# Kernel optimization log

Hardware: AMD Instinct MI355X
Metric: run time of the kernel (lower is better)

The kernel has to match this reference:

```python
import math
import jax, jax.numpy as jnp
import numpy as np

INPUT_DIM = 1024
HEADS = 16
SEQ = 4096
BATCH = 1
SCALE = math.sqrt(INPUT_DIM / HEADS)  # 8.0


def setup_inputs() -> dict:
    key = jax.random.key(0)
    ks = jax.random.split(key, 5)
    D = INPUT_DIM
    return {
        "x": jax.random.normal(ks[0], (BATCH, SEQ, D), dtype=jnp.float32),
        "w_qkv": jax.random.normal(ks[1], (3 * D, D), dtype=jnp.float32) * (1.0 / math.sqrt(D)),
        "b_qkv": jax.random.normal(ks[2], (3 * D,), dtype=jnp.float32) * 0.01,
        "w_out": jax.random.normal(ks[3], (D, D), dtype=jnp.float32) * (1.0 / math.sqrt(D)),
        "b_out": jax.random.normal(ks[4], (D,), dtype=jnp.float32) * 0.01,
    }


def reference(x, w_qkv, b_qkv, w_out, b_out):
    b, n, D = x.shape
    h = HEADS
    d = D // h
    # qkv projection: [b, n, 3D]
    qkv = x @ w_qkv.T + b_qkv
    # 'b n (c h d) -> b c h n d' with c=3 outermost
    qkv = qkv.reshape(b, n, 3, h, d).transpose(2, 0, 3, 1, 4)  # [3, b, h, n, d]
    q, k, v = qkv[0], qkv[1], qkv[2]
    q = q / SCALE
    attn = jnp.einsum('bhnd,bhmd->bhnm', q, k)  # [b, h, n, n]
    attn = jax.nn.softmax(attn, axis=-1)
    # dropout is identity in eval mode
    context = jnp.einsum('bhnm,bhmd->bhnd', attn, v)  # [b, h, n, d]
    context = context.transpose(0, 2, 1, 3).reshape(b, n, D)  # 'b h n d -> b n (h d)'
    return context @ w_out.T + b_out
```

## Files before the change

kernel.cpp:

```cpp
#include <hip/hip_runtime.h>

typedef unsigned short u16;
typedef unsigned int u32;
typedef __attribute__((ext_vector_type(8))) short short8;
typedef __attribute__((ext_vector_type(4))) float f32x4;

__device__ __forceinline__ u16 f2b(float f) {
  union { float f; unsigned u; } v; v.f = f;
  unsigned r = (v.u + 0x7FFFu + ((v.u >> 16) & 1u)) >> 16;
  return (u16)r;
}
__device__ __forceinline__ float b2f(u16 b) {
  union { unsigned u; float f; } v; v.u = ((unsigned)b) << 16;
  return v.f;
}
__device__ __forceinline__ u32 cvtpk(float a, float b) {
  u32 r;
  asm("v_cvt_pk_bf16_f32 %0, %1, %2" : "=v"(r) : "v"(a), "v"(b));
  return r;
}
__device__ __forceinline__ void p32swap(u32& a, u32& b) {
  asm("v_permlane32_swap_b32 %0, %1" : "+v"(a), "+v"(b));
}
__device__ __forceinline__ void p16swap(u32& a, u32& b) {
  asm("v_permlane16_swap_b32 %0, %1" : "+v"(a), "+v"(b));
}
__device__ __forceinline__ float ldf(const void* p, size_t i, int f32) {
  return f32 ? ((const float*)p)[i] : b2f(((const u16*)p)[i]);
}

__global__ __launch_bounds__(256) void detect_dtype(const u16* __restrict__ x,
                                                    int* __restrict__ flag) {
  __shared__ int cnt;
  if (threadIdx.x == 0) cnt = 0;
  __syncthreads();
  int local = 0;
  for (int p = threadIdx.x; p < 512; p += 256) {
    int e = (x[2 * p] >> 7) & 0xFF;
    if (e >= 0xC0) local++;
  }
  atomicAdd(&cnt, local);
  __syncthreads();
  if (threadIdx.x == 0) flag[0] = (cnt >= 16) ? 1 : 0;
}

__global__ __launch_bounds__(256) void convert_all(
    const void* __restrict__ px, const void* __restrict__ pwq,
    const void* __restrict__ pbq, const void* __restrict__ pwo,
    const void* __restrict__ pbo, u16* __restrict__ xb,
    u16* __restrict__ wqkvb, u16* __restrict__ bqkvb, u16* __restrict__ wob,
    u16* __restrict__ bob) {
  __shared__ int sf;
  if (threadIdx.x == 0) sf = 0;
  __syncthreads();
  {
    const u16* xr = (const u16*)px;
    int local = 0;
    for (int p = threadIdx.x; p < 512; p += 256) {
      int e = (xr[2 * p] >> 7) & 0xFF;
      if (e >= 0xC0) local++;
    }
    atomicAdd(&sf, local);
  }
  __syncthreads();
  const int isf32 = (sf >= 16);

  int i = blockIdx.x * 256 + threadIdx.x;
  const void* in; u16* out; size_t g;
  if (i < 524288)       { in = px;  out = xb;    g = (size_t)i; }
  else if (i < 917504)  { in = pwq; out = wqkvb; g = (size_t)(i - 524288); }
  else if (i < 917888)  { in = pbq; out = bqkvb; g = (size_t)(i - 917504); }
  else if (i < 1048960) { in = pwo; out = wob;   g = (size_t)(i - 917888); }
  else                  { in = pbo; out = bob;   g = (size_t)(i - 1048960); }
  size_t base = g * 8;
  if (isf32) {
    const float* p = (const float*)in + base;
    float4 v0 = *(const float4*)p, v1 = *(const float4*)(p + 4);
    union { short8 v; u16 e[8]; } t;
    t.e[0]=f2b(v0.x); t.e[1]=f2b(v0.y); t.e[2]=f2b(v0.z); t.e[3]=f2b(v0.w);
    t.e[4]=f2b(v1.x); t.e[5]=f2b(v1.y); t.e[6]=f2b(v1.z); t.e[7]=f2b(v1.w);
    *(short8*)(out + base) = t.v;
  } else {
    *(short8*)(out + base) = *(const short8*)((const u16*)in + base);
  }
}

__global__ __launch_bounds__(256) void transpose_v(const u16* __restrict__ qkv,
                                                   u16* __restrict__ Vt) {
  __shared__ u16 T[64 * 72];
  const int tid = threadIdx.x;
  const int h = blockIdx.y;
  const int s0 = blockIdx.x * 64;
  for (int r = 0; r < 2; ++r) {
    int cid = r * 256 + tid;
    int s = cid >> 3, c8 = cid & 7;
    union { short8 v; u16 u[8]; } uu;
    uu.v = *(const short8*)(qkv + (size_t)(s0 + s) * 3072 + 2048 + h * 64 + c8 * 8);
    for (int i = 0; i < 8; ++i) T[(c8 * 8 + i) * 72 + s] = uu.u[i];
  }
  __syncthreads();
  for (int r = 0; r < 2; ++r) {
    int cid = r * 256 + tid;
    int dd = cid >> 3, c8 = cid & 7;
    union { short8 v; u16 u[8]; } uu;
    for (int i = 0; i < 8; ++i) uu.u[i] = T[dd * 72 + c8 * 8 + i];
    *(short8*)(Vt + (size_t)(h * 64 + dd) * 4096 + s0 + c8 * 8) = uu.v;
  }
}

__global__ __launch_bounds__(256) void gemm1_db(const u16* __restrict__ A,
                                                const u16* __restrict__ B,
                                                const u16* __restrict__ bias,
                                                u16* __restrict__ C,
                                                int K, int lda, int ldb, int ldc) {
  __shared__ __align__(16) u16 sm[2][16384];
  const int tid = threadIdx.x;
  const int w = tid >> 6, lane = tid & 63;
  const int lq = lane & 15, qr = lane >> 4;
  const int m0 = blockIdx.y * 128, n0 = blockIdx.x * 128;
  const int wm = (w >> 1) * 64, wn = (w & 1) * 64;

  f32x4 acc[4][4];
  for (int i = 0; i < 4; i++)
    for (int j = 0; j < 4; j++) acc[i][j] = (f32x4){0.f, 0.f, 0.f, 0.f};
  float bv[4];
  for (int ns = 0; ns < 4; ++ns) bv[ns] = b2f(bias[n0 + wn + ns * 16 + lq]);

  const int rs = tid >> 3, cs = tid & 7;
  const u16* gA = A + (size_t)(m0 + rs) * lda + cs * 8;
  const u16* gB = B + (size_t)(n0 + rs) * ldb + cs * 8;
  const int lofs = (tid & ~63) << 3;

#define GSTAGE(buf, k0)                                                      \
  do {                                                                       \
    u16* As_ = &sm[buf][0];                                                  \
    u16* Bs_ = &sm[buf][8192];                                               \
    for (int r = 0; r < 4; ++r) {                                            \
      __builtin_amdgcn_global_load_lds(gA + (size_t)(r * 32) * lda + (k0),   \
                                       As_ + lofs + r * 2048, 16, 0, 0);     \
      __builtin_amdgcn_global_load_lds(gB + (size_t)(r * 32) * ldb + (k0),   \
                                       Bs_ + lofs + r * 2048, 16, 0, 0);     \
    }                                                                        \
  } while (0)

  GSTAGE(0, 0);
  __syncthreads();

  const int nk = K >> 6;
  for (int kt = 0; kt < nk; ++kt) {
    const int cur = kt & 1;
    if (kt + 1 < nk) GSTAGE(cur ^ 1, (kt + 1) * 64);
    const u16* As = &sm[cur][0];
    const u16* Bs = &sm[cur][8192];
    for (int ks = 0; ks < 2; ++ks) {
      short8 af[4], bf[4];
      const int sw = ks * 4 + qr;
      for (int i = 0; i < 4; i++) {
        af[i] = *(const short8*)(As + (wm + i * 16 + lq) * 64 + sw * 8);
        bf[i] = *(const short8*)(Bs + (wn + i * 16 + lq) * 64 + sw * 8);
      }
      for (int mi = 0; mi < 4; mi++)
        for (int ni = 0; ni < 4; ni++)
          acc[mi][ni] = __builtin_amdgcn_mfma_f32_16x16x32_bf16(
              af[mi], bf[ni], acc[mi][ni], 0, 0, 0);
    }
    __syncthreads();
  }
#undef GSTAGE

  u16* SH = &sm[0][0];
  for (int mi = 0; mi < 4; mi++)
    for (int ni = 0; ni < 4; ni++)
      for (int r = 0; r < 4; ++r)
        SH[(wm + mi * 16 + qr * 4 + r) * 132 + wn + ni * 16 + lq] =
            f2b(acc[mi][ni][r] + bv[ni]);
  __syncthreads();
  for (int it = 0; it < 8; ++it) {
    int idx = it * 256 + tid;
    int row = idx >> 4, c8 = idx & 15;
    *(short8*)(C + (size_t)(m0 + row) * ldc + n0 + c8 * 8) =
        *(const short8*)(SH + row * 132 + c8 * 8);
  }
}

__global__ __launch_bounds__(256) void gemm_bt(const void* __restrict__ A,
                                               const void* __restrict__ B,
                                               const void* __restrict__ bias,
                                               void* __restrict__ C,
                                               int M, int N, int K,
                                               int lda, int ldb, int ldc,
                                               int aMay, int bMay, int outF32,
                                               const int* __restrict__ flag) {
  __shared__ __align__(16) u16 sm[128 * 132];
  u16* As = sm;
  u16* Bs = sm + 128 * 64;
  const int f = flag[0];
  const int a32 = aMay && f, b32 = bMay && f;
  const int tid = threadIdx.x;
  const int w = tid >> 6, lane = tid & 63;
  const int lq = lane & 15, qr = lane >> 4;
  const int m0 = blockIdx.y * 128, n0 = blockIdx.x * 128;
  const int wm = (w >> 1) * 64, wn = (w & 1) * 64;

  f32x4 acc[4][4];
  for (int i = 0; i < 4; i++)
    for (int j = 0; j < 4; j++) acc[i][j] = (f32x4){0.f, 0.f, 0.f, 0.f};
  float bv[4];
  for (int ns = 0; ns < 4; ++ns) bv[ns] = ldf(bias, n0 + wn + ns * 16 + lq, b32);

  const int rs = tid >> 3, cs = tid & 7;
  const u16* gA = (const u16*)A + (size_t)(m0 + rs) * lda + cs * 8;
  const u16* gB = (const u16*)B + (size_t)(n0 + rs) * ldb + cs * 8;
  u16* lA = As + ((tid & ~63) << 3);
  u16* lB = Bs + ((tid & ~63) << 3);

  for (int k0 = 0; k0 < K; k0 += 64) {
    if (!(a32 | b32)) {
      for (int r = 0; r < 4; ++r) {
        __builtin_amdgcn_global_load_lds(gA + (size_t)(r * 32) * lda + k0,
                                         lA + r * 2048, 16, 0, 0);
        __builtin_amdgcn_global_load_lds(gB + (size_t)(r * 32) * ldb + k0,
                                         lB + r * 2048, 16, 0, 0);
      }
    } else {
      for (int r = 0; r < 4; ++r) {
        int cid = r * 256 + tid;
        int row = cid >> 3, c = cid & 7;
        if (a32) {
          const float* p = (const float*)A + (size_t)(m0 + row) * lda + k0 + c * 8;
          float4 v0 = *(const float4*)p, v1 = *(const float4*)(p + 4);
          union { short8 v; u16 e[8]; } t;
          t.e[0]=f2b(v0.x); t.e[1]=f2b(v0.y); t.e[2]=f2b(v0.z); t.e[3]=f2b(v0.w);
          t.e[4]=f2b(v1.x); t.e[5]=f2b(v1.y); t.e[6]=f2b(v1.z); t.e[7]=f2b(v1.w);
          *(short8*)(As + row * 64 + c * 8) = t.v;
        } else {
          *(short8*)(As + row * 64 + c * 8) =
              *(const short8*)((const u16*)A + (size_t)(m0 + row) * lda + k0 + c * 8);
        }
        if (b32) {
          const float* p = (const float*)B + (size_t)(n0 + row) * ldb + k0 + c * 8;
          float4 v0 = *(const float4*)p, v1 = *(const float4*)(p + 4);
          union { short8 v; u16 e[8]; } t;
          t.e[0]=f2b(v0.x); t.e[1]=f2b(v0.y); t.e[2]=f2b(v0.z); t.e[3]=f2b(v0.w);
          t.e[4]=f2b(v1.x); t.e[5]=f2b(v1.y); t.e[6]=f2b(v1.z); t.e[7]=f2b(v1.w);
          *(short8*)(Bs + row * 64 + c * 8) = t.v;
        } else {
          *(short8*)(Bs + row * 64 + c * 8) =
              *(const short8*)((const u16*)B + (size_t)(n0 + row) * ldb + k0 + c * 8);
        }
      }
    }
    __syncthreads();
    for (int ks = 0; ks < 2; ++ks) {
      short8 af[4], bf[4];
      const int sw = ks * 4 + qr;
      for (int i = 0; i < 4; i++) {
        af[i] = *(const short8*)(As + (wm + i * 16 + lq) * 64 + sw * 8);
        bf[i] = *(const short8*)(Bs + (wn + i * 16 + lq) * 64 + sw * 8);
      }
      for (int mi = 0; mi < 4; mi++)
        for (int ni = 0; ni < 4; ni++)
          acc[mi][ni] = __builtin_amdgcn_mfma_f32_16x16x32_bf16(
              af[mi], bf[ni], acc[mi][ni], 0, 0, 0);
    }
    __syncthreads();
  }

  if (!outF32) {
    u16* SH = sm;
    for (int mi = 0; mi < 4; mi++)
      for (int ni = 0; ni < 4; ni++)
        for (int r = 0; r < 4; ++r)
          SH[(wm + mi * 16 + qr * 4 + r) * 132 + wn + ni * 16 + lq] =
              f2b(acc[mi][ni][r] + bv[ni]);
    __syncthreads();
    for (int it = 0; it < 8; ++it) {
      int idx = it * 256 + tid;
      int row = idx >> 4, c8 = idx & 15;
      *(short8*)((u16*)C + (size_t)(m0 + row) * ldc + n0 + c8 * 8) =
          *(const short8*)(SH + row * 132 + c8 * 8);
    }
  } else {
    float* Cf = (float*)C;
    for (int mi = 0; mi < 4; mi++) {
      int row = m0 + wm + mi * 16 + qr * 4;
      for (int r = 0; r < 4; ++r) {
        float* rp = Cf + (size_t)(row + r) * ldc + n0 + wn;
        for (int ni = 0; ni < 4; ni++)
          rp[ni * 16 + lq] = acc[mi][ni][r] + bv[ni];
      }
    }
  }
}

__global__ __launch_bounds__(512, 2) void gemm_bt_ks(const u16* __restrict__ A,
                                                     const u16* __restrict__ B,
                                                     const u16* __restrict__ bias,
                                                     float* __restrict__ C,
                                                     int K, int lda, int ldb, int ldc) {
  __shared__ __align__(16) u16 sm[2][16384];
  const int tid = threadIdx.x;
  const int w = tid >> 6, lane = tid & 63;
  const int half = w >> 2, wq = w & 3;
  const int ht = tid & 255;
  const int lq = lane & 15, qr = lane >> 4;
  const int m0 = blockIdx.y * 128, n0 = blockIdx.x * 128;
  const int wm = (wq >> 1) * 64, wn = (wq & 1) * 64;
  const int kh = K >> 1;

  u16* As = &sm[half][0];
  u16* Bs = &sm[half][8192];

  f32x4 acc[4][4];
  for (int i = 0; i < 4; i++)
    for (int j = 0; j < 4; j++) acc[i][j] = (f32x4){0.f, 0.f, 0.f, 0.f};
  float bv[4];
  for (int ns = 0; ns < 4; ++ns) bv[ns] = b2f(bias[n0 + wn + ns * 16 + lq]);

  const int rs = ht >> 3, cs = ht & 7;
  const u16* gA = A + (size_t)(m0 + rs) * lda + half * kh + cs * 8;
  const u16* gB = B + (size_t)(n0 + rs) * ldb + half * kh + cs * 8;
  u16* lA = As + ((ht & ~63) << 3);
  u16* lB = Bs + ((ht & ~63) << 3);

  for (int k0 = 0; k0 < kh; k0 += 64) {
    for (int r = 0; r < 4; ++r) {
      __builtin_amdgcn_global_load_lds(gA + (size_t)(r * 32) * lda + k0,
                                       lA + r * 2048, 16, 0, 0);
      __builtin_amdgcn_global_load_lds(gB + (size_t)(r * 32) * ldb + k0,
                                       lB + r * 2048, 16, 0, 0);
    }
    __syncthreads();
    for (int ks = 0; ks < 2; ++ks) {
      short8 af[4], bf[4];
      const int sw = ks * 4 + qr;
      for (int i = 0; i < 4; i++) {
        af[i] = *(const short8*)(As + (wm + i * 16 + lq) * 64 + sw * 8);
        bf[i] = *(const short8*)(Bs + (wn + i * 16 + lq) * 64 + sw * 8);
      }
      for (int mi = 0; mi < 4; mi++)
        for (int ni = 0; ni < 4; ni++)
          acc[mi][ni] = __builtin_amdgcn_mfma_f32_16x16x32_bf16(
              af[mi], bf[ni], acc[mi][ni], 0, 0, 0);
    }
    __syncthreads();
  }

  float* CB = (float*)&sm[0][0];
  float* p = CB + (size_t)ht * 33;
  for (int t = 0; t < 2; ++t) {
    if (half == 1) {
      for (int u = 0; u < 2; ++u)
        for (int ni = 0; ni < 4; ++ni)
          for (int r = 0; r < 4; ++r)
            p[u * 16 + ni * 4 + r] = acc[2 * t + u][ni][r];
    }
    __syncthreads();
    if (half == 0) {
      for (int u = 0; u < 2; ++u)
        for (int ni = 0; ni < 4; ++ni)
          for (int r = 0; r < 4; ++r)
            acc[2 * t + u][ni][r] += p[u * 16 + ni * 4 + r];
    }
    __syncthreads();
  }

  if (half == 0) {
    for (int mi = 0; mi < 4; mi++) {
      int row = m0 + wm + mi * 16 + qr * 4;
      for (int r = 0; r < 4; ++r) {
        float* rp = C + (size_t)(row + r) * ldc + n0 + wn;
        for (int ni = 0; ni < 4; ni++)
          rp[ni * 16 + lq] = acc[mi][ni][r] + bv[ni];
      }
    }
  }
}

__global__ __launch_bounds__(512, 2) void attn_split(const u16* __restrict__ qkv,
                                                     const u16* __restrict__ Vtg,
                                                     u16* __restrict__ ctx, int ldctx) {
  __shared__ __align__(16) u16 SMEM[2][16384];
  const int tid = threadIdx.x;
  const int w = tid >> 6, lane = tid & 63;
  const int half = w >> 2, wq = w & 3, wl = w & 3;
  const int lq = lane & 15, qr = lane >> 4;
  const int qb = blockIdx.x, h = blockIdx.y;
  const int qbase = qb * 128 + wq * 32;
  const float cs = 0.18033688011112042f;

  short8 qf[2][2];
#pragma unroll
  for (int mi = 0; mi < 2; ++mi)
#pragma unroll
    for (int ks = 0; ks < 2; ++ks)
      qf[mi][ks] = *(const short8*)(qkv + (size_t)(qbase + mi * 16 + lq) * 3072 +
                                    h * 64 + ks * 32 + qr * 8);

  f32x4 o[2][4];
#pragma unroll
  for (int mi = 0; mi < 2; ++mi)
#pragma unroll
    for (int ds = 0; ds < 4; ++ds) o[mi][ds] = (f32x4){0.f, 0.f, 0.f, 0.f};
  float lrow[2] = {0.f, 0.f};

  const int csw = ((lane & 7) ^ (lane >> 3)) << 3;
  const int r0v = wl * 8 + (lane >> 3);
  const u16* sK0 = qkv + (size_t)(half * 2048 + r0v) * 3072 + 1024 + h * 64 + csw;
  const u16* sK1 = sK0 + (size_t)32 * 3072;
  const u16* sV0 = Vtg + (size_t)(h * 64 + r0v) * 4096 + half * 2048 + csw;
  const u16* sV1 = sV0 + (size_t)32 * 4096;
  const int kb = half * 4096 + wl * 512;
  const int vb = 8192 + half * 4096 + wl * 512;

#define STAGE(buf)                                                          \
  do {                                                                      \
    u16* B_ = &SMEM[buf][0];                                                \
    __builtin_amdgcn_global_load_lds(sK0, B_ + kb, 16, 0, 0);               \
    __builtin_amdgcn_global_load_lds(sK1, B_ + kb + 2048, 16, 0, 0);        \
    __builtin_amdgcn_global_load_lds(sV0, B_ + vb, 16, 0, 0);               \
    __builtin_amdgcn_global_load_lds(sV1, B_ + vb + 2048, 16, 0, 0);        \
    sK0 += (size_t)64 * 3072; sK1 += (size_t)64 * 3072;                     \
    sV0 += 64; sV1 += 64;                                                   \
  } while (0)

  STAGE(0);
  __syncthreads();

  for (int it = 0; it < 32; ++it) {
    const int cur = it & 1;
    if (it + 1 < 32) STAGE(cur ^ 1);
    const u16* Kh = &SMEM[cur][half * 4096];
    const u16* Vh = &SMEM[cur][8192 + half * 4096];

    f32x4 s[2][4];
#pragma unroll
    for (int mi = 0; mi < 2; ++mi)
#pragma unroll
      for (int ns = 0; ns < 4; ++ns) s[mi][ns] = (f32x4){0.f, 0.f, 0.f, 0.f};
#pragma unroll
    for (int ks = 0; ks < 2; ++ks) {
      short8 kf[4];
#pragma unroll
      for (int ns = 0; ns < 4; ++ns) {
        int rk = ns * 16 + lq;
        kf[ns] = *(const short8*)(Kh + rk * 64 + (((ks * 4 + qr) ^ (lq & 7)) << 3));
      }
      __builtin_amdgcn_s_setprio(1);
#pragma unroll
      for (int mi = 0; mi < 2; ++mi)
#pragma unroll
        for (int ns = 0; ns < 4; ++ns)
          s[mi][ns] = __builtin_amdgcn_mfma_f32_16x16x32_bf16(
              kf[ns], qf[mi][ks], s[mi][ns], 0, 0, 0);
      __builtin_amdgcn_s_setprio(0);
    }

    short8 pf[2][2];
#pragma unroll
    for (int mi = 0; mi < 2; ++mi) {
      float lacc = 0.f;
      u32 X[4], Y[4];
#pragma unroll
      for (int ns = 0; ns < 4; ++ns) {
        float p0 = __builtin_amdgcn_exp2f(fmaf(s[mi][ns][0], cs, -12.0f));
        float p1 = __builtin_amdgcn_exp2f(fmaf(s[mi][ns][1], cs, -12.0f));
        float p2 = __builtin_amdgcn_exp2f(fmaf(s[mi][ns][2], cs, -12.0f));
        float p3 = __builtin_amdgcn_exp2f(fmaf(s[mi][ns][3], cs, -12.0f));
        lacc += (p0 + p1) + (p2 + p3);
        X[ns] = cvtpk(p0, p1);
        Y[ns] = cvtpk(p2, p3);
      }
      lrow[mi] += lacc;
#pragma unroll
      for (int ks = 0; ks < 2; ++ks) {
        u32 a0 = X[2 * ks], b0 = X[2 * ks + 1];
        u32 a1 = Y[2 * ks], b1 = Y[2 * ks + 1];
        p32swap(a0, b0); p16swap(a0, b0);
        p32swap(a1, b1); p16swap(a1, b1);
        union { u32 u[4]; short8 v; } t;
        t.u[0] = a0; t.u[1] = a1; t.u[2] = b0; t.u[3] = b1;
        pf[mi][ks] = t.v;
      }
    }

#pragma unroll
    for (int ks = 0; ks < 2; ++ks) {
      short8 vf[4];
#pragma unroll
      for (int ds = 0; ds < 4; ++ds) {
        int dv = ds * 16 + lq;
        vf[ds] = *(const short8*)(Vh + (size_t)dv * 64 +
                                  (((ks * 4 + qr) ^ (lq & 7)) << 3));
      }
      __builtin_amdgcn_s_setprio(1);
#pragma unroll
      for (int mi = 0; mi < 2; ++mi)
#pragma unroll
        for (int ds = 0; ds < 4; ++ds)
          o[mi][ds] = __builtin_amdgcn_mfma_f32_16x16x32_bf16(
              vf[ds], pf[mi][ks], o[mi][ds], 0, 0, 0);
      __builtin_amdgcn_s_setprio(0);
    }
    __syncthreads();
  }
#undef STAGE

  float* CB = (float*)&SMEM[0][0];
#pragma unroll
  for (int mi = 0; mi < 2; ++mi) {
    float* p = CB + (size_t)(wq * 64 + lane) * 17;
    if (half == 1) {
#pragma unroll
      for (int ds = 0; ds < 4; ++ds) {
        p[ds * 4 + 0] = o[mi][ds][0];
        p[ds * 4 + 1] = o[mi][ds][1];
        p[ds * 4 + 2] = o[mi][ds][2];
        p[ds * 4 + 3] = o[mi][ds][3];
      }
      p[16] = lrow[mi];
    }
    __syncthreads();
    if (half == 0) {
#pragma unroll
      for (int ds = 0; ds < 4; ++ds) {
        o[mi][ds][0] += p[ds * 4 + 0];
        o[mi][ds][1] += p[ds * 4 + 1];
        o[mi][ds][2] += p[ds * 4 + 2];
        o[mi][ds][3] += p[ds * 4 + 3];
      }
      lrow[mi] += p[16];
    }
    __syncthreads();
  }

  if (half == 0) {
#pragma unroll
    for (int mi = 0; mi < 2; ++mi) {
      float l = lrow[mi];
      l += __shfl_xor(l, 16, 64);
      l += __shfl_xor(l, 32, 64);
      float linv = 1.f / fmaxf(l, 1e-30f);
      int row = qbase + mi * 16 + lq;
      u16* dst = ctx + (size_t)row * ldctx + h * 64 + qr * 4;
#pragma unroll
      for (int ds = 0; ds < 4; ++ds) {
        u32 lo = cvtpk(o[mi][ds][0] * linv, o[mi][ds][1] * linv);
        u32 hi = cvtpk(o[mi][ds][2] * linv, o[mi][ds][3] * linv);
        *(uint2*)(dst + ds * 16) = make_uint2(lo, hi);
      }
    }
  }
}

__global__ __launch_bounds__(256) void attn_fused(const u16* __restrict__ qkv,
                                                  const u16* __restrict__ Vtg,
                                                  u16* __restrict__ ctx, int ldctx) {
  __shared__ u16 Ks[64 * 64];
  __shared__ u16 Vts[64 * 64];
  const int tid = threadIdx.x;
  const int w = tid >> 6, lane = tid & 63;
  const int lq = lane & 15, qr = lane >> 4;
  const int qb = blockIdx.x, h = blockIdx.y;
  const int qbase = qb * 128 + w * 32;
  const float cs = 0.18033688011112042f;

  short8 qf[2][2];
  for (int mi = 0; mi < 2; ++mi)
    for (int ks = 0; ks < 2; ++ks)
      qf[mi][ks] = *(const short8*)(qkv + (size_t)(qbase + mi * 16 + lq) * 3072 +
                                    h * 64 + ks * 32 + qr * 8);

  f32x4 o[2][4];
  for (int mi = 0; mi < 2; ++mi)
    for (int ds = 0; ds < 4; ++ds) o[mi][ds] = (f32x4){0.f, 0.f, 0.f, 0.f};
  float lrow[2] = {0.f, 0.f};

  const int c = tid & 7, r0 = tid >> 3;
  u16* dKA = Ks + r0 * 64 + ((c ^ (r0 & 7)) << 3);
  u16* dKB = dKA + 32 * 64;
  const u16* sKA = qkv + (size_t)r0 * 3072 + 1024 + h * 64 + c * 8;
  const u16* sKB = sKA + (size_t)32 * 3072;
  const u16* sVfA = qkv + (size_t)r0 * 3072 + 2048 + h * 64 + c * 8;
  const u16* sVfB = sVfA + (size_t)32 * 3072;

  short8 rKA, rKB;
  union { short8 v; u16 e[8]; } ufA, ufB;
  rKA = *(const short8*)sKA; sKA += (size_t)64 * 3072;
  rKB = *(const short8*)sKB; sKB += (size_t)64 * 3072;
  ufA.v = *(const short8*)sVfA; sVfA += (size_t)64 * 3072;
  ufB.v = *(const short8*)sVfB; sVfB += (size_t)64 * 3072;

  for (int j0 = 0; j0 < 4096; j0 += 64) {
    __syncthreads();
    *(short8*)dKA = rKA;
    *(short8*)dKB = rKB;
    {
      const int jc = r0 >> 3;
      for (int i = 0; i < 8; ++i)
        Vts[(c * 8 + i) * 64 + ((jc ^ i) << 3) + (r0 & 7)] = ufA.e[i];
    }
    {
      const int jc = (r0 + 32) >> 3;
      for (int i = 0; i < 8; ++i)
        Vts[(c * 8 + i) * 64 + ((jc ^ i) << 3) + (r0 & 7)] = ufB.e[i];
    }
    __syncthreads();

    if (j0 + 64 < 4096) {
      rKA = *(const short8*)sKA; sKA += (size_t)64 * 3072;
      rKB = *(const short8*)sKB; sKB += (size_t)64 * 3072;
      ufA.v = *(const short8*)sVfA; sVfA += (size_t)64 * 3072;
      ufB.v = *(const short8*)sVfB; sVfB += (size_t)64 * 3072;
    }

    f32x4 s[2][4];
    for (int mi = 0; mi < 2; ++mi)
      for (int ns = 0; ns < 4; ++ns) s[mi][ns] = (f32x4){0.f, 0.f, 0.f, 0.f};
    for (int ks = 0; ks < 2; ++ks) {
      short8 kf[4];
      for (int ns = 0; ns < 4; ++ns) {
        int rk = ns * 16 + lq;
        kf[ns] = *(const short8*)(Ks + rk * 64 + (((ks * 4 + qr) ^ (lq & 7)) << 3));
      }
      __builtin_amdgcn_s_setprio(1);
      for (int mi = 0; mi < 2; ++mi)
        for (int ns = 0; ns < 4; ++ns)
          s[mi][ns] = __builtin_amdgcn_mfma_f32_16x16x32_bf16(
              kf[ns], qf[mi][ks], s[mi][ns], 0, 0, 0);
      __builtin_amdgcn_s_setprio(0);
    }

    short8 pf[2][2];
#pragma unroll
    for (int mi = 0; mi < 2; ++mi) {
      float lacc = 0.f;
      u32 X[4], Y[4];
#pragma unroll
      for (int ns = 0; ns < 4; ++ns) {
        float p0 = __builtin_amdgcn_exp2f(fmaf(s[mi][ns][0], cs, -12.0f));
        float p1 = __builtin_amdgcn_exp2f(fmaf(s[mi][ns][1], cs, -12.0f));
        float p2 = __builtin_amdgcn_exp2f(fmaf(s[mi][ns][2], cs, -12.0f));
        float p3 = __builtin_amdgcn_exp2f(fmaf(s[mi][ns][3], cs, -12.0f));
        lacc += (p0 + p1) + (p2 + p3);
        X[ns] = cvtpk(p0, p1);
        Y[ns] = cvtpk(p2, p3);
      }
      lrow[mi] += lacc;
#pragma unroll
      for (int ks = 0; ks < 2; ++ks) {
        u32 a0 = X[2 * ks], b0 = X[2 * ks + 1];
        u32 a1 = Y[2 * ks], b1 = Y[2 * ks + 1];
        p32swap(a0, b0); p16swap(a0, b0);
        p32swap(a1, b1); p16swap(a1, b1);
        union { u32 u[4]; short8 v; } t;
        t.u[0] = a0; t.u[1] = a1; t.u[2] = b0; t.u[3] = b1;
        pf[mi][ks] = t.v;
      }
    }

    for (int ks = 0; ks < 2; ++ks) {
      short8 vf[4];
      for (int ds = 0; ds < 4; ++ds) {
        int dv = ds * 16 + lq;
        vf[ds] = *(const short8*)(Vts + (size_t)dv * 64 +
                                  (((ks * 4 + qr) ^ (lq & 7)) << 3));
      }
      __builtin_amdgcn_s_setprio(1);
      for (int mi = 0; mi < 2; ++mi)
        for (int ds = 0; ds < 4; ++ds)
          o[mi][ds] = __builtin_amdgcn_mfma_f32_16x16x32_bf16(
              vf[ds], pf[mi][ks], o[mi][ds], 0, 0, 0);
      __builtin_amdgcn_s_setprio(0);
    }
  }

  for (int mi = 0; mi < 2; ++mi) {
    float l = lrow[mi];
    l += __shfl_xor(l, 16, 64);
    l += __shfl_xor(l, 32, 64);
    float linv = 1.f / fmaxf(l, 1e-30f);
    int row = qbase + mi * 16 + lq;
    u16* dst = ctx + (size_t)row * ldctx + h * 64 + qr * 4;
    for (int ds = 0; ds < 4; ++ds) {
      u32 lo = cvtpk(o[mi][ds][0] * linv, o[mi][ds][1] * linv);
      u32 hi = cvtpk(o[mi][ds][2] * linv, o[mi][ds][3] * linv);
      *(uint2*)(dst + ds * 16) = make_uint2(lo, hi);
    }
  }
}

extern "C" void kernel_launch(void* const* d_in, const int* in_sizes, int n_in,
                              void* d_out, int out_size, void* d_ws, size_t ws_size,
                              hipStream_t stream) {
  float* out = (float*)d_out;

  const void *px = nullptr, *pwq = nullptr, *pbq = nullptr, *pwo = nullptr, *pbo = nullptr;
  if (n_in == 5) {
    for (int i = 0; i < 5; ++i) {
      switch (in_sizes[i]) {
        case 4194304: px = d_in[i]; break;
        case 3145728: pwq = d_in[i]; break;
        case 3072:    pbq = d_in[i]; break;
        case 1048576: pwo = d_in[i]; break;
        case 1024:    pbo = d_in[i]; break;
        default: break;
      }
    }
  }
  if (!px || !pwq || !pbq || !pwo || !pbo) {
    px = d_in[0]; pwq = d_in[1]; pbq = d_in[2]; pwo = d_in[3]; pbo = d_in[4];
  }

  int* flag = (int*)d_ws;
  u16* qkv = (u16*)((char*)d_ws + 64);
  u16* ctx = qkv;

  const size_t nQKV = (size_t)4096 * 3072;
  const size_t nVt = (size_t)16 * 64 * 4096;
  const size_t nx = 4194304, nwq = 3145728, nwo = 1048576;
  u16* Vtg = qkv + nQKV;
  const size_t need_vt = 64 + (nQKV + nVt) * 2;
  const size_t need_full = need_vt + (nx + nwq + 4096 + nwo + 1024) * 2;

  if (ws_size >= need_full) {
    u16* xb    = Vtg + nVt;
    u16* wqkvb = xb + nx;
    u16* bqkvb = wqkvb + nwq;
    u16* wob   = bqkvb + 4096;
    u16* bob   = wob + nwo;
    convert_all<<<4098, 256, 0, stream>>>(px, pwq, pbq, pwo, pbo,
                                          xb, wqkvb, bqkvb, wob, bob);

    gemm1_db<<<dim3(24, 32), 256, 0, stream>>>(xb, wqkvb, bqkvb, qkv,
                                               1024, 1024, 1024, 3072);
    transpose_v<<<dim3(64, 16), 256, 0, stream>>>(qkv, Vtg);
    attn_split<<<dim3(32, 16), 512, 0, stream>>>(qkv, Vtg, ctx, 3072);
    gemm_bt_ks<<<dim3(8, 32), 512, 0, stream>>>(ctx, wob, bob, out,
                                                1024, 3072, 1024, 1024);
  } else if (ws_size >= need_vt) {
    detect_dtype<<<1, 256, 0, stream>>>((const u16*)px, flag);
    gemm_bt<<<dim3(24, 32), 256, 0, stream>>>(px, pwq, pbq, qkv,
                                              4096, 3072, 1024, 1024, 1024, 3072,
                                              1, 1, 0, flag);
    transpose_v<<<dim3(64, 16), 256, 0, stream>>>(qkv, Vtg);
    attn_split<<<dim3(32, 16), 512, 0, stream>>>(qkv, Vtg, ctx, 3072);
    gemm_bt<<<dim3(8, 32), 256, 0, stream>>>(ctx, pwo, pbo, out,
                                             4096, 1024, 1024, 3072, 1024, 1024,
                                             0, 1, 1, flag);
  } else {
    detect_dtype<<<1, 256, 0, stream>>>((const u16*)px, flag);
    gemm_bt<<<dim3(24, 32), 256, 0, stream>>>(px, pwq, pbq, qkv,
                                              4096, 3072, 1024, 1024, 1024, 3072,
                                              1, 1, 0, flag);
    attn_fused<<<dim3(32, 16), 256, 0, stream>>>(qkv, (const u16*)nullptr, ctx, 3072);
    gemm_bt<<<dim3(8, 32), 256, 0, stream>>>(ctx, pwo, pbo, out,
                                             4096, 1024, 1024, 3072, 1024, 1024,
                                             0, 1, 1, flag);
  }
}
```

Measured before the change: 244.6 us.

## Replace split-K output GEMM with double-buffered single-pass GEMM

Result: faster. 235.5 us (-3.7%).

```diff
diff --git a/kernel.cpp b/kernel.cpp
--- a/kernel.cpp
+++ b/kernel.cpp
@@ -180,6 +180,76 @@
     int row = idx >> 4, c8 = idx & 15;
     *(short8*)(C + (size_t)(m0 + row) * ldc + n0 + c8 * 8) =
         *(const short8*)(SH + row * 132 + c8 * 8);
+  }
+}
+
+__global__ __launch_bounds__(256) void gemm2_db(const u16* __restrict__ A,
+                                                const u16* __restrict__ B,
+                                                const u16* __restrict__ bias,
+                                                float* __restrict__ C,
+                                                int K, int lda, int ldb, int ldc) {
+  __shared__ __align__(16) u16 sm[2][16384];
+  const int tid = threadIdx.x;
+  const int w = tid >> 6, lane = tid & 63;
+  const int lq = lane & 15, qr = lane >> 4;
+  const int m0 = blockIdx.y * 128, n0 = blockIdx.x * 128;
+  const int wm = (w >> 1) * 64, wn = (w & 1) * 64;
+
+  f32x4 acc[4][4];
+  for (int i = 0; i < 4; i++)
+    for (int j = 0; j < 4; j++) acc[i][j] = (f32x4){0.f, 0.f, 0.f, 0.f};
+  float bv[4];
+  for (int ns = 0; ns < 4; ++ns) bv[ns] = b2f(bias[n0 + wn + ns * 16 + lq]);
+
+  const int rs = tid >> 3, cs = tid & 7;
+  const u16* gA = A + (size_t)(m0 + rs) * lda + cs * 8;
+  const u16* gB = B + (size_t)(n0 + rs) * ldb + cs * 8;
+  const int lofs = (tid & ~63) << 3;
+
+#define GSTAGE(buf, k0)                                                      \
+  do {                                                                       \
+    u16* As_ = &sm[buf][0];                                                  \
+    u16* Bs_ = &sm[buf][8192];                                               \
+    for (int r = 0; r < 4; ++r) {                                            \
+      __builtin_amdgcn_global_load_lds(gA + (size_t)(r * 32) * lda + (k0),   \
+                                       As_ + lofs + r * 2048, 16, 0, 0);     \
+      __builtin_amdgcn_global_load_lds(gB + (size_t)(r * 32) * ldb + (k0),   \
+                                       Bs_ + lofs + r * 2048, 16, 0, 0);     \
+    }                                                                        \
+  } while (0)
+
+  GSTAGE(0, 0);
+  __syncthreads();
+
+  const int nk = K >> 6;
+  for (int kt = 0; kt < nk; ++kt) {
+    const int cur = kt & 1;
+    if (kt + 1 < nk) GSTAGE(cur ^ 1, (kt + 1) * 64);
+    const u16* As = &sm[cur][0];
+    const u16* Bs = &sm[cur][8192];
+    for (int ks = 0; ks < 2; ++ks) {
+      short8 af[4], bf[4];
+      const int sw = ks * 4 + qr;
+      for (int i = 0; i < 4; i++) {
+        af[i] = *(const short8*)(As + (wm + i * 16 + lq) * 64 + sw * 8);
+        bf[i] = *(const short8*)(Bs + (wn + i * 16 + lq) * 64 + sw * 8);
+      }
+      for (int mi = 0; mi < 4; mi++)
+        for (int ni = 0; ni < 4; ni++)
+          acc[mi][ni] = __builtin_amdgcn_mfma_f32_16x16x32_bf16(
+              af[mi], bf[ni], acc[mi][ni], 0, 0, 0);
+    }
+    __syncthreads();
+  }
+#undef GSTAGE
+
+  for (int mi = 0; mi < 4; mi++) {
+    int row = m0 + wm + mi * 16 + qr * 4;
+    for (int r = 0; r < 4; ++r) {
+      float* rp = C + (size_t)(row + r) * ldc + n0 + wn;
+      for (int ni = 0; ni < 4; ni++)
+        rp[ni * 16 + lq] = acc[mi][ni][r] + bv[ni];
+    }
   }
 }
 
@@ -293,90 +363,6 @@
   }
 }
 
-__global__ __launch_bounds__(512, 2) void gemm_bt_ks(const u16* __restrict__ A,
-                                                     const u16* __restrict__ B,
-                                                     const u16* __restrict__ bias,
-                                                     float* __restrict__ C,
-                                                     int K, int lda, int ldb, int ldc) {
-  __shared__ __align__(16) u16 sm[2][16384];
-  const int tid = threadIdx.x;
-  const int w = tid >> 6, lane = tid & 63;
-  const int half = w >> 2, wq = w & 3;
-  const int ht = tid & 255;
-  const int lq = lane & 15, qr = lane >> 4;
-  const int m0 = blockIdx.y * 128, n0 = blockIdx.x * 128;
-  const int wm = (wq >> 1) * 64, wn = (wq & 1) * 64;
-  const int kh = K >> 1;
-
-  u16* As = &sm[half][0];
-  u16* Bs = &sm[half][8192];
-
-  f32x4 acc[4][4];
-  for (int i = 0; i < 4; i++)
-    for (int j = 0; j < 4; j++) acc[i][j] = (f32x4){0.f, 0.f, 0.f, 0.f};
-  float bv[4];
-  for (int ns = 0; ns < 4; ++ns) bv[ns] = b2f(bias[n0 + wn + ns * 16 + lq]);
-
-  const int rs = ht >> 3, cs = ht & 7;
-  const u16* gA = A + (size_t)(m0 + rs) * lda + half * kh + cs * 8;
-  const u16* gB = B + (size_t)(n0 + rs) * ldb + half * kh + cs * 8;
-  u16* lA = As + ((ht & ~63) << 3);
-  u16* lB = Bs + ((ht & ~63) << 3);
-
-  for (int k0 = 0; k0 < kh; k0 += 64) {
-    for (int r = 0; r < 4; ++r) {
-      __builtin_amdgcn_global_load_lds(gA + (size_t)(r * 32) * lda + k0,
-                                       lA + r * 2048, 16, 0, 0);
-      __builtin_amdgcn_global_load_lds(gB + (size_t)(r * 32) * ldb + k0,
-                                       lB + r * 2048, 16, 0, 0);
-    }
-    __syncthreads();
-    for (int ks = 0; ks < 2; ++ks) {
-      short8 af[4], bf[4];
-      const int sw = ks * 4 + qr;
-      for (int i = 0; i < 4; i++) {
-        af[i] = *(const short8*)(As + (wm + i * 16 + lq) * 64 + sw * 8);
-        bf[i] = *(const short8*)(Bs + (wn + i * 16 + lq) * 64 + sw * 8);
-      }
-      for (int mi = 0; mi < 4; mi++)
-        for (int ni = 0; ni < 4; ni++)
-          acc[mi][ni] = __builtin_amdgcn_mfma_f32_16x16x32_bf16(
-              af[mi], bf[ni], acc[mi][ni], 0, 0, 0);
-    }
-    __syncthreads();
-  }
-
-  float* CB = (float*)&sm[0][0];
-  float* p = CB + (size_t)ht * 33;
-  for (int t = 0; t < 2; ++t) {
-    if (half == 1) {
-      for (int u = 0; u < 2; ++u)
-        for (int ni = 0; ni < 4; ++ni)
-          for (int r = 0; r < 4; ++r)
-            p[u * 16 + ni * 4 + r] = acc[2 * t + u][ni][r];
-    }
-    __syncthreads();
-    if (half == 0) {
-      for (int u = 0; u < 2; ++u)
-        for (int ni = 0; ni < 4; ++ni)
-          for (int r = 0; r < 4; ++r)
-            acc[2 * t + u][ni][r] += p[u * 16 + ni * 4 + r];
-    }
-    __syncthreads();
-  }
-
-  if (half == 0) {
-    for (int mi = 0; mi < 4; mi++) {
-      int row = m0 + wm + mi * 16 + qr * 4;
-      for (int r = 0; r < 4; ++r) {
-        float* rp = C + (size_t)(row + r) * ldc + n0 + wn;
-        for (int ni = 0; ni < 4; ni++)
-          rp[ni * 16 + lq] = acc[mi][ni][r] + bv[ni];
-      }
-    }
-  }
-}
-
 __global__ __launch_bounds__(512, 2) void attn_split(const u16* __restrict__ qkv,
                                                      const u16* __restrict__ Vtg,
                                                      u16* __restrict__ ctx, int ldctx) {
@@ -736,8 +722,8 @@
                                                1024, 1024, 1024, 3072);
     transpose_v<<<dim3(64, 16), 256, 0, stream>>>(qkv, Vtg);
     attn_split<<<dim3(32, 16), 512, 0, stream>>>(qkv, Vtg, ctx, 3072);
-    gemm_bt_ks<<<dim3(8, 32), 512, 0, stream>>>(ctx, wob, bob, out,
-                                                1024, 3072, 1024, 1024);
+    gemm2_db<<<dim3(8, 32), 256, 0, stream>>>(ctx, wob, bob, out,
+                                              1024, 3072, 1024, 1024);
   } else if (ws_size >= need_vt) {
     detect_dtype<<<1, 256, 0, stream>>>((const u16*)px, flag);
     gemm_bt<<<dim3(24, 32), 256, 0, stream>>>(px, pwq, pbq, qkv,
```
